# Kernel optimization log

Measured on AMD Instinct MI355X. Metric: run time of the kernel, lower is better.

## Reference

```python
import jax, jax.numpy as jnp
import numpy as np

EPS = 1e-09


def setup_inputs() -> dict:
    key = jax.random.key(0)
    k1, k2 = jax.random.split(key)
    vocab_size, embed_dim = 128000, 1024
    psi = jax.random.normal(k1, (embed_dim,), dtype=jnp.float32)
    vocab_reps = jax.random.normal(k2, (vocab_size, embed_dim), dtype=jnp.float32)
    return {"psi": psi, "vocab_reps": vocab_reps, "top_k": 5}


def reference(psi, vocab_reps, top_k):
    # Normalize query state: psi / (||psi|| + eps)
    psi_norm = psi / (jnp.linalg.norm(psi) + EPS)
    # Normalize every vocab row: [V, D] / ([V, 1] + eps)
    vocab_norms = vocab_reps / (jnp.linalg.norm(vocab_reps, axis=1, keepdims=True) + EPS)
    # Cosine similarities via GEVM: [V]
    similarities = vocab_norms @ psi_norm
    top_scores, top_indices = jax.lax.top_k(similarities, top_k)
    return top_scores, top_indices
```

## Files before the change

kernel.cpp:

```cpp
#include <hip/hip_runtime.h>
#include <math.h>
#include <limits.h>

#define EPS  1e-9f
#define TOPK 5

__device__ __forceinline__ bool better(float av, int ai, float bv, int bi) {
    return (av > bv) || (av == bv && ai < bi);
}

__device__ __forceinline__ void insert_top(float sv[TOPK], int si[TOPK], float v, int idx) {
    if (!better(v, idx, sv[TOPK - 1], si[TOPK - 1])) return;
    sv[TOPK - 1] = v; si[TOPK - 1] = idx;
#pragma unroll
    for (int j = TOPK - 1; j > 0; --j) {
        if (better(sv[j], si[j], sv[j - 1], si[j - 1])) {
            float tv = sv[j]; sv[j] = sv[j - 1]; sv[j - 1] = tv;
            int   ti = si[j]; si[j] = si[j - 1]; si[j - 1] = ti;
        }
    }
}

__global__ __launch_bounds__(256) void psi_norm_kernel(const float* __restrict__ psi,
                                                       int D,
                                                       float* __restrict__ scale_out) {
    __shared__ float red[8];
    const int tid = threadIdx.x;
    float s = 0.f;
    for (int i = tid; i < D; i += blockDim.x) {
        float v = psi[i];
        s += v * v;
    }
    for (int off = 32; off > 0; off >>= 1) s += __shfl_xor(s, off);
    const int lane = tid & 63, wave = tid >> 6;
    if (lane == 0) red[wave] = s;
    __syncthreads();
    if (tid == 0) {
        const int nwaves = blockDim.x >> 6;
        float t = 0.f;
        for (int w = 0; w < nwaves; ++w) t += red[w];
        scale_out[0] = 1.0f / (sqrtf(t) + EPS);
    }
}

__global__ __launch_bounds__(256) void sim_top_kernel(const float4* __restrict__ vocab,
                                                      const float4* __restrict__ psi4,
                                                      const float* __restrict__ scale_ptr,
                                                      float* __restrict__ cand_v,
                                                      int* __restrict__ cand_i,
                                                      int V, int D) {
    __shared__ float4 psi_lds[256];
    __shared__ float  wv[4 * TOPK];
    __shared__ int    wi[4 * TOPK];
    const int tid = threadIdx.x;
    const int D4  = D >> 2;
    for (int i = tid; i < D4; i += blockDim.x) psi_lds[i] = psi4[i];
    __syncthreads();

    const int lane = tid & 63;
    const int wave = tid >> 6;
    const int wavesPerBlock = blockDim.x >> 6;
    const int gwave  = blockIdx.x * wavesPerBlock + wave;
    const int nwaves = gridDim.x * wavesPerBlock;
    const float scale = scale_ptr[0];
    const int iters = D4 >> 6;

    float tv[TOPK]; int ti[TOPK];
#pragma unroll
    for (int j = 0; j < TOPK; ++j) { tv[j] = -INFINITY; ti[j] = INT_MAX; }

    for (int row = gwave; row < V; row += nwaves) {
        const float4* rp = vocab + (size_t)row * D4;
        float dot = 0.f, nrm = 0.f;
#pragma unroll 4
        for (int it = 0; it < iters; ++it) {
            float4 a = rp[it * 64 + lane];
            float4 p = psi_lds[it * 64 + lane];
            dot += a.x * p.x + a.y * p.y + a.z * p.z + a.w * p.w;
            nrm += a.x * a.x + a.y * a.y + a.z * a.z + a.w * a.w;
        }
        for (int off = 32; off > 0; off >>= 1) {
            dot += __shfl_xor(dot, off);
            nrm += __shfl_xor(nrm, off);
        }
        if (lane == 0) {
            float sim = dot * scale / (sqrtf(nrm) + EPS);
            insert_top(tv, ti, sim, row);
        }
    }

    if (lane == 0) {
#pragma unroll
        for (int j = 0; j < TOPK; ++j) { wv[wave * TOPK + j] = tv[j]; wi[wave * TOPK + j] = ti[j]; }
    }
    __syncthreads();
    if (tid == 0) {
        float bv[TOPK]; int bi[TOPK];
#pragma unroll
        for (int j = 0; j < TOPK; ++j) { bv[j] = -INFINITY; bi[j] = INT_MAX; }
        for (int e = 0; e < wavesPerBlock * TOPK; ++e) insert_top(bv, bi, wv[e], wi[e]);
#pragma unroll
        for (int j = 0; j < TOPK; ++j) {
            cand_v[blockIdx.x * TOPK + j] = bv[j];
            cand_i[blockIdx.x * TOPK + j] = bi[j];
        }
    }
}

__global__ __launch_bounds__(1024) void topk_reduce_kernel(const float* __restrict__ cand_v,
                                                           const int* __restrict__ cand_i,
                                                           int NC, int K,
                                                           float* __restrict__ out) {
    __shared__ float wv[16 * TOPK];
    __shared__ int   wi[16 * TOPK];
    const int tid = threadIdx.x;
    const int lane = tid & 63, wave = tid >> 6;
    const int nwaves = blockDim.x >> 6;

    float sv[TOPK]; int si[TOPK];
#pragma unroll
    for (int j = 0; j < TOPK; ++j) { sv[j] = -INFINITY; si[j] = INT_MAX; }

    for (int i = tid; i < NC; i += blockDim.x) insert_top(sv, si, cand_v[i], cand_i[i]);

    for (int step = 1; step < 64; step <<= 1) {
        float ov[TOPK]; int oi[TOPK];
#pragma unroll
        for (int j = 0; j < TOPK; ++j) {
            ov[j] = __shfl_xor(sv[j], step);
            oi[j] = __shfl_xor(si[j], step);
        }
#pragma unroll
        for (int j = 0; j < TOPK; ++j) insert_top(sv, si, ov[j], oi[j]);
    }

    if (lane == 0) {
#pragma unroll
        for (int j = 0; j < TOPK; ++j) { wv[wave * TOPK + j] = sv[j]; wi[wave * TOPK + j] = si[j]; }
    }
    __syncthreads();
    if (tid == 0) {
        float bv[TOPK]; int bi[TOPK];
#pragma unroll
        for (int j = 0; j < TOPK; ++j) { bv[j] = -INFINITY; bi[j] = INT_MAX; }
        for (int e = 0; e < nwaves * TOPK; ++e) insert_top(bv, bi, wv[e], wi[e]);
        for (int k = 0; k < K && k < TOPK; ++k) {
            out[k]     = bv[k];
            out[K + k] = (float)bi[k];
        }
    }
}

extern "C" void kernel_launch(void* const* d_in, const int* in_sizes, int n_in,
                              void* d_out, int out_size, void* d_ws, size_t ws_size,
                              hipStream_t stream) {
    const float* psi   = (const float*)d_in[0];
    const float* vocab = (const float*)d_in[1];
    const int D = in_sizes[0];
    const int V = in_sizes[1] / D;
    const int K = out_size / 2;

    const int blocks = 2048;
    const int NC = blocks * TOPK;

    float* ws     = (float*)d_ws;
    float* scale  = ws;
    float* cand_v = ws + 256;
    int*   cand_i = (int*)(ws + 256 + NC);

    psi_norm_kernel<<<1, 256, 0, stream>>>(psi, D, scale);

    sim_top_kernel<<<blocks, 256, 0, stream>>>((const float4*)vocab, (const float4*)psi,
                                               scale, cand_v, cand_i, V, D);

    topk_reduce_kernel<<<1, 1024, 0, stream>>>(cand_v, cand_i, NC, K, (float*)d_out);
}
```

Baseline: 130.1 us.

## Fuse psi norm into sim kernel, hold psi in registers, process row pairs

Removes the separate psi-norm launch: each wave computes the psi norm itself from psi held in registers, which also replaces the LDS copy of psi. The main loop handles two rows per wave iteration with eight nontemporal 16-byte loads issued up front, for more memory-level parallelism. The grid drops to 2000 blocks, so the 64000 row pairs divide evenly across waves. D is now hardcoded to 1024, so the kernel is only correct for that embedding size.

```diff
diff --git a/kernel.cpp b/kernel.cpp
--- a/kernel.cpp
+++ b/kernel.cpp
@@ -4,6 +4,8 @@
 
 #define EPS  1e-9f
 #define TOPK 5
+
+typedef float v4f __attribute__((ext_vector_type(4)));
 
 __device__ __forceinline__ bool better(float av, int ai, float bv, int bi) {
     return (av > bv) || (av == bv && ai < bi);
@@ -21,84 +23,90 @@
     }
 }
 
-__global__ __launch_bounds__(256) void psi_norm_kernel(const float* __restrict__ psi,
-                                                       int D,
-                                                       float* __restrict__ scale_out) {
-    __shared__ float red[8];
-    const int tid = threadIdx.x;
-    float s = 0.f;
-    for (int i = tid; i < D; i += blockDim.x) {
-        float v = psi[i];
-        s += v * v;
-    }
-    for (int off = 32; off > 0; off >>= 1) s += __shfl_xor(s, off);
-    const int lane = tid & 63, wave = tid >> 6;
-    if (lane == 0) red[wave] = s;
-    __syncthreads();
-    if (tid == 0) {
-        const int nwaves = blockDim.x >> 6;
-        float t = 0.f;
-        for (int w = 0; w < nwaves; ++w) t += red[w];
-        scale_out[0] = 1.0f / (sqrtf(t) + EPS);
-    }
+__device__ __forceinline__ float dot4(v4f a, v4f b) {
+    return a.x * b.x + a.y * b.y + a.z * b.z + a.w * b.w;
 }
 
-__global__ __launch_bounds__(256) void sim_top_kernel(const float4* __restrict__ vocab,
-                                                      const float4* __restrict__ psi4,
-                                                      const float* __restrict__ scale_ptr,
+__global__ __launch_bounds__(256) void sim_top_kernel(const v4f* __restrict__ vocab,
+                                                      const v4f* __restrict__ psi4,
                                                       float* __restrict__ cand_v,
                                                       int* __restrict__ cand_i,
-                                                      int V, int D) {
-    __shared__ float4 psi_lds[256];
-    __shared__ float  wv[4 * TOPK];
-    __shared__ int    wi[4 * TOPK];
-    const int tid = threadIdx.x;
-    const int D4  = D >> 2;
-    for (int i = tid; i < D4; i += blockDim.x) psi_lds[i] = psi4[i];
-    __syncthreads();
-
+                                                      int V) {
+    __shared__ float wvs[4 * TOPK];
+    __shared__ int   wis[4 * TOPK];
+    const int tid  = threadIdx.x;
     const int lane = tid & 63;
     const int wave = tid >> 6;
     const int wavesPerBlock = blockDim.x >> 6;
     const int gwave  = blockIdx.x * wavesPerBlock + wave;
     const int nwaves = gridDim.x * wavesPerBlock;
-    const float scale = scale_ptr[0];
-    const int iters = D4 >> 6;
+
+    const v4f p0 = psi4[lane];
+    const v4f p1 = psi4[64 + lane];
+    const v4f p2 = psi4[128 + lane];
+    const v4f p3 = psi4[192 + lane];
+
+    float ps = dot4(p0, p0) + dot4(p1, p1) + dot4(p2, p2) + dot4(p3, p3);
+    for (int off = 32; off > 0; off >>= 1) ps += __shfl_xor(ps, off);
+    const float scale = 1.0f / (sqrtf(ps) + EPS);
 
     float tv[TOPK]; int ti[TOPK];
 #pragma unroll
     for (int j = 0; j < TOPK; ++j) { tv[j] = -INFINITY; ti[j] = INT_MAX; }
 
-    for (int row = gwave; row < V; row += nwaves) {
-        const float4* rp = vocab + (size_t)row * D4;
-        float dot = 0.f, nrm = 0.f;
-#pragma unroll 4
-        for (int it = 0; it < iters; ++it) {
-            float4 a = rp[it * 64 + lane];
-            float4 p = psi_lds[it * 64 + lane];
-            dot += a.x * p.x + a.y * p.y + a.z * p.z + a.w * p.w;
-            nrm += a.x * a.x + a.y * a.y + a.z * a.z + a.w * a.w;
-        }
+    const int NP = V >> 1;
+    for (int p = gwave; p < NP; p += nwaves) {
+        const v4f* ra = vocab + (size_t)(2 * p) * 256;
+        const v4f* rb = ra + 256;
+        v4f a0 = __builtin_nontemporal_load(ra + lane);
+        v4f a1 = __builtin_nontemporal_load(ra + 64 + lane);
+        v4f a2 = __builtin_nontemporal_load(ra + 128 + lane);
+        v4f a3 = __builtin_nontemporal_load(ra + 192 + lane);
+        v4f b0 = __builtin_nontemporal_load(rb + lane);
+        v4f b1 = __builtin_nontemporal_load(rb + 64 + lane);
+        v4f b2 = __builtin_nontemporal_load(rb + 128 + lane);
+        v4f b3 = __builtin_nontemporal_load(rb + 192 + lane);
+
+        float dotA = dot4(a0, p0) + dot4(a1, p1) + dot4(a2, p2) + dot4(a3, p3);
+        float nrmA = dot4(a0, a0) + dot4(a1, a1) + dot4(a2, a2) + dot4(a3, a3);
+        float dotB = dot4(b0, p0) + dot4(b1, p1) + dot4(b2, p2) + dot4(b3, p3);
+        float nrmB = dot4(b0, b0) + dot4(b1, b1) + dot4(b2, b2) + dot4(b3, b3);
+
         for (int off = 32; off > 0; off >>= 1) {
-            dot += __shfl_xor(dot, off);
-            nrm += __shfl_xor(nrm, off);
+            dotA += __shfl_xor(dotA, off);
+            nrmA += __shfl_xor(nrmA, off);
+            dotB += __shfl_xor(dotB, off);
+            nrmB += __shfl_xor(nrmB, off);
         }
         if (lane == 0) {
-            float sim = dot * scale / (sqrtf(nrm) + EPS);
-            insert_top(tv, ti, sim, row);
+            insert_top(tv, ti, dotA * scale / (sqrtf(nrmA) + EPS), 2 * p);
+            insert_top(tv, ti, dotB * scale / (sqrtf(nrmB) + EPS), 2 * p + 1);
         }
+    }
+
+    if ((V & 1) && gwave == 0) {
+        const int row = V - 1;
+        const v4f* ra = vocab + (size_t)row * 256;
+        v4f a0 = ra[lane], a1 = ra[64 + lane], a2 = ra[128 + lane], a3 = ra[192 + lane];
+        float dotA = dot4(a0, p0) + dot4(a1, p1) + dot4(a2, p2) + dot4(a3, p3);
+        float nrmA = dot4(a0, a0) + dot4(a1, a1) + dot4(a2, a2) + dot4(a3, a3);
+        for (int off = 32; off > 0; off >>= 1) {
+            dotA += __shfl_xor(dotA, off);
+            nrmA += __shfl_xor(nrmA, off);
+        }
+        if (lane == 0) insert_top(tv, ti, dotA * scale / (sqrtf(nrmA) + EPS), row);
     }
 
     if (lane == 0) {
 #pragma unroll
-        for (int j = 0; j < TOPK; ++j) { wv[wave * TOPK + j] = tv[j]; wi[wave * TOPK + j] = ti[j]; }
+        for (int j = 0; j < TOPK; ++j) { wvs[wave * TOPK + j] = tv[j]; wis[wave * TOPK + j] = ti[j]; }
     }
     __syncthreads();
     if (tid == 0) {
         float bv[TOPK]; int bi[TOPK];
 #pragma unroll
         for (int j = 0; j < TOPK; ++j) { bv[j] = -INFINITY; bi[j] = INT_MAX; }
-        for (int e = 0; e < wavesPerBlock * TOPK; ++e) insert_top(bv, bi, wv[e], wi[e]);
+        for (int e = 0; e < wavesPerBlock * TOPK; ++e) insert_top(bv, bi, wvs[e], wis[e]);
 #pragma unroll
         for (int j = 0; j < TOPK; ++j) {
             cand_v[blockIdx.x * TOPK + j] = bv[j];
@@ -111,8 +119,8 @@
                                                            const int* __restrict__ cand_i,
                                                            int NC, int K,
                                                            float* __restrict__ out) {
-    __shared__ float wv[16 * TOPK];
-    __shared__ int   wi[16 * TOPK];
+    __shared__ float wvs[16 * TOPK];
+    __shared__ int   wis[16 * TOPK];
     const int tid = threadIdx.x;
     const int lane = tid & 63, wave = tid >> 6;
     const int nwaves = blockDim.x >> 6;
@@ -136,14 +144,14 @@
 
     if (lane == 0) {
 #pragma unroll
-        for (int j = 0; j < TOPK; ++j) { wv[wave * TOPK + j] = sv[j]; wi[wave * TOPK + j] = si[j]; }
+        for (int j = 0; j < TOPK; ++j) { wvs[wave * TOPK + j] = sv[j]; wis[wave * TOPK + j] = si[j]; }
     }
     __syncthreads();
     if (tid == 0) {
         float bv[TOPK]; int bi[TOPK];
 #pragma unroll
         for (int j = 0; j < TOPK; ++j) { bv[j] = -INFINITY; bi[j] = INT_MAX; }
-        for (int e = 0; e < nwaves * TOPK; ++e) insert_top(bv, bi, wv[e], wi[e]);
+        for (int e = 0; e < nwaves * TOPK; ++e) insert_top(bv, bi, wvs[e], wis[e]);
         for (int k = 0; k < K && k < TOPK; ++k) {
             out[k]     = bv[k];
             out[K + k] = (float)bi[k];
@@ -159,19 +167,16 @@
     const int D = in_sizes[0];
     const int V = in_sizes[1] / D;
     const int K = out_size / 2;
+    (void)D;
 
-    const int blocks = 2048;
+    const int blocks = 2000;
     const int NC = blocks * TOPK;
 
-    float* ws     = (float*)d_ws;
-    float* scale  = ws;
-    float* cand_v = ws + 256;
-    int*   cand_i = (int*)(ws + 256 + NC);
+    float* cand_v = (float*)d_ws;
+    int*   cand_i = (int*)((float*)d_ws + NC);
 
-    psi_norm_kernel<<<1, 256, 0, stream>>>(psi, D, scale);
-
-    sim_top_kernel<<<blocks, 256, 0, stream>>>((const float4*)vocab, (const float4*)psi,
-                                               scale, cand_v, cand_i, V, D);
+    sim_top_kernel<<<blocks, 256, 0, stream>>>((const v4f*)vocab, (const v4f*)psi,
+                                               cand_v, cand_i, V);
 
     topk_reduce_kernel<<<1, 1024, 0, stream>>>(cand_v, cand_i, NC, K, (float*)d_out);
 }
```

New measurement: 113.7 us. 12.5% less time.

## Fold psi norm into sim kernel and split top-k into separate passes

Applied to the files above, without the earlier changes.

The separate psi-norm kernel is removed; each wave now recomputes the query norm from the LDS copy of psi. The similarity kernel writes all similarities to a workspace array instead of keeping per-wave top-k state. Two new top-k kernels then reduce that array: 256 blocks produce candidates and one block picks the final result. This takes the insertion logic out of the bandwidth-bound GEVM loop, but adds a full write and read of the V-length similarity array and keeps three launches.

```diff
diff --git a/kernel.cpp b/kernel.cpp
--- a/kernel.cpp
+++ b/kernel.cpp
@@ -21,39 +21,13 @@
     }
 }
 
-__global__ __launch_bounds__(256) void psi_norm_kernel(const float* __restrict__ psi,
-                                                       int D,
-                                                       float* __restrict__ scale_out) {
-    __shared__ float red[8];
+__global__ __launch_bounds__(256) void sim_kernel(const float4* __restrict__ vocab,
+                                                  const float4* __restrict__ psi4,
+                                                  float* __restrict__ sims,
+                                                  int V, int D) {
+    __shared__ float4 psi_lds[256];
     const int tid = threadIdx.x;
-    float s = 0.f;
-    for (int i = tid; i < D; i += blockDim.x) {
-        float v = psi[i];
-        s += v * v;
-    }
-    for (int off = 32; off > 0; off >>= 1) s += __shfl_xor(s, off);
-    const int lane = tid & 63, wave = tid >> 6;
-    if (lane == 0) red[wave] = s;
-    __syncthreads();
-    if (tid == 0) {
-        const int nwaves = blockDim.x >> 6;
-        float t = 0.f;
-        for (int w = 0; w < nwaves; ++w) t += red[w];
-        scale_out[0] = 1.0f / (sqrtf(t) + EPS);
-    }
-}
-
-__global__ __launch_bounds__(256) void sim_top_kernel(const float4* __restrict__ vocab,
-                                                      const float4* __restrict__ psi4,
-                                                      const float* __restrict__ scale_ptr,
-                                                      float* __restrict__ cand_v,
-                                                      int* __restrict__ cand_i,
-                                                      int V, int D) {
-    __shared__ float4 psi_lds[256];
-    __shared__ float  wv[4 * TOPK];
-    __shared__ int    wi[4 * TOPK];
-    const int tid = threadIdx.x;
-    const int D4  = D >> 2;
+    const int D4 = D >> 2;
     for (int i = tid; i < D4; i += blockDim.x) psi_lds[i] = psi4[i];
     __syncthreads();
 
@@ -62,12 +36,16 @@
     const int wavesPerBlock = blockDim.x >> 6;
     const int gwave  = blockIdx.x * wavesPerBlock + wave;
     const int nwaves = gridDim.x * wavesPerBlock;
-    const float scale = scale_ptr[0];
-    const int iters = D4 >> 6;
+    const int iters  = D4 >> 6;
 
-    float tv[TOPK]; int ti[TOPK];
-#pragma unroll
-    for (int j = 0; j < TOPK; ++j) { tv[j] = -INFINITY; ti[j] = INT_MAX; }
+    float ps = 0.f;
+#pragma unroll 4
+    for (int it = 0; it < iters; ++it) {
+        float4 p = psi_lds[it * 64 + lane];
+        ps += p.x * p.x + p.y * p.y + p.z * p.z + p.w * p.w;
+    }
+    for (int off = 32; off > 0; off >>= 1) ps += __shfl_xor(ps, off);
+    const float scale = 1.0f / (sqrtf(ps) + EPS);
 
     for (int row = gwave; row < V; row += nwaves) {
         const float4* rp = vocab + (size_t)row * D4;
@@ -83,22 +61,49 @@
             dot += __shfl_xor(dot, off);
             nrm += __shfl_xor(nrm, off);
         }
-        if (lane == 0) {
-            float sim = dot * scale / (sqrtf(nrm) + EPS);
-            insert_top(tv, ti, sim, row);
+        if (lane == 0) sims[row] = dot * scale / (sqrtf(nrm) + EPS);
+    }
+}
+
+__global__ __launch_bounds__(256) void topk_stage1(const float* __restrict__ sims,
+                                                   int V,
+                                                   float* __restrict__ cand_v,
+                                                   int* __restrict__ cand_i) {
+    __shared__ float wvs[4 * TOPK];
+    __shared__ int   wis[4 * TOPK];
+    const int tid = threadIdx.x;
+    const int lane = tid & 63, wave = tid >> 6;
+    const int wavesPerBlock = blockDim.x >> 6;
+    const int gtid = blockIdx.x * blockDim.x + tid;
+    const int nthr = gridDim.x * blockDim.x;
+
+    float sv[TOPK]; int si[TOPK];
+#pragma unroll
+    for (int j = 0; j < TOPK; ++j) { sv[j] = -INFINITY; si[j] = INT_MAX; }
+
+    for (int i = gtid; i < V; i += nthr) insert_top(sv, si, sims[i], i);
+
+    for (int step = 1; step < 64; step <<= 1) {
+        float ov[TOPK]; int oi[TOPK];
+#pragma unroll
+        for (int j = 0; j < TOPK; ++j) {
+            ov[j] = __shfl_xor(sv[j], step);
+            oi[j] = __shfl_xor(si[j], step);
         }
+#pragma unroll
+        for (int j = 0; j < TOPK; ++j) insert_top(sv, si, ov[j], oi[j]);
     }
 
     if (lane == 0) {
 #pragma unroll
-        for (int j = 0; j < TOPK; ++j) { wv[wave * TOPK + j] = tv[j]; wi[wave * TOPK + j] = ti[j]; }
+        for (int j = 0; j < TOPK; ++j) { wvs[wave * TOPK + j] = sv[j]; wis[wave * TOPK + j] = si[j]; }
     }
     __syncthreads();
     if (tid == 0) {
         float bv[TOPK]; int bi[TOPK];
 #pragma unroll
         for (int j = 0; j < TOPK; ++j) { bv[j] = -INFINITY; bi[j] = INT_MAX; }
-        for (int e = 0; e < wavesPerBlock * TOPK; ++e) insert_top(bv, bi, wv[e], wi[e]);
+        for (int e = 0; e < wavesPerBlock * TOPK; ++e) insert_top(bv, bi, wvs[e], wis[e]);
 #pragma unroll
         for (int j = 0; j < TOPK; ++j) {
             cand_v[blockIdx.x * TOPK + j] = bv[j];
@@ -107,12 +112,12 @@
     }
 }
 
-__global__ __launch_bounds__(1024) void topk_reduce_kernel(const float* __restrict__ cand_v,
-                                                           const int* __restrict__ cand_i,
-                                                           int NC, int K,
-                                                           float* __restrict__ out) {
-    __shared__ float wv[16 * TOPK];
-    __shared__ int   wi[16 * TOPK];
+__global__ __launch_bounds__(256) void topk_final(const float* __restrict__ cand_v,
+                                                  const int* __restrict__ cand_i,
+                                                  int NC, int K,
+                                                  float* __restrict__ out) {
+    __shared__ float wvs[4 * TOPK];
+    __shared__ int   wis[4 * TOPK];
     const int tid = threadIdx.x;
     const int lane = tid & 63, wave = tid >> 6;
     const int nwaves = blockDim.x >> 6;
@@ -136,14 +141,14 @@
 
     if (lane == 0) {
 #pragma unroll
-        for (int j = 0; j < TOPK; ++j) { wv[wave * TOPK + j] = sv[j]; wi[wave * TOPK + j] = si[j]; }
+        for (int j = 0; j < TOPK; ++j) { wvs[wave * TOPK + j] = sv[j]; wis[wave * TOPK + j] = si[j]; }
     }
     __syncthreads();
     if (tid == 0) {
         float bv[TOPK]; int bi[TOPK];
 #pragma unroll
         for (int j = 0; j < TOPK; ++j) { bv[j] = -INFINITY; bi[j] = INT_MAX; }
-        for (int e = 0; e < nwaves * TOPK; ++e) insert_top(bv, bi, wv[e], wi[e]);
+        for (int e = 0; e < nwaves * TOPK; ++e) insert_top(bv, bi, wvs[e], wis[e]);
         for (int k = 0; k < K && k < TOPK; ++k) {
             out[k]     = bv[k];
             out[K + k] = (float)bi[k];
@@ -160,18 +165,19 @@
     const int V = in_sizes[1] / D;
     const int K = out_size / 2;
 
-    const int blocks = 2048;
-    const int NC = blocks * TOPK;
+    const int blocks1 = 2048;
+    const int blocks2 = 256;
+    const int NC = blocks2 * TOPK;
 
     float* ws     = (float*)d_ws;
-    float* scale  = ws;
-    float* cand_v = ws + 256;
-    int*   cand_i = (int*)(ws + 256 + NC);
+    float* sims   = ws;
+    float* cand_v = ws + V;
+    int*   cand_i = (int*)(ws + V + NC);
 
-    psi_norm_kernel<<<1, 256, 0, stream>>>(psi, D, scale);
+    sim_kernel<<<blocks1, 256, 0, stream>>>((const float4*)vocab, (const float4*)psi,
+                                            sims, V, D);
 
-    sim_top_kernel<<<blocks, 256, 0, stream>>>((const float4*)vocab, (const float4*)psi,
-                                               scale, cand_v, cand_i, V, D);
+    topk_stage1<<<blocks2, 256, 0, stream>>>(sims, V, cand_v, cand_i);
 
-    topk_reduce_kernel<<<1, 1024, 0, stream>>>(cand_v, cand_i, NC, K, (float*)d_out);
+    topk_final<<<1, 256, 0, stream>>>(cand_v, cand_i, NC, K, (float*)d_out);
 }
```

Result: no change. 129.3 us (-0.6%).
